# Optimization experiments

Measured on AMD Instinct MI355X. Metric: run time of the kernel, lower is better.

## Reference

```python
import jax, jax.numpy as jnp
import numpy as np

Nc, Ns, Nt, d_h, BS = 64, 64, 64, 128, 16


def setup_inputs() -> dict:
    key = jax.random.key(0)
    k1, k2, k3, k4, k5 = jax.random.split(key, 5)
    Ac = (jax.random.uniform(k1, (Ns, Nc)) < 0.05).astype(jnp.float32)
    As = (jax.random.uniform(k2, (Ns, Ns)) < 0.05).astype(jnp.float32)
    # AA = As@As@Ac + As@Ac + Ac, then binarize (masked_fill(AA != 0, 1))
    AA = As @ As @ Ac + As @ Ac + Ac
    AA = (AA != 0).astype(jnp.float32)                 # [Ns, Nc]
    AA_mask = jnp.tile(AA, (Nt, Nt))                   # [Ns*Nt, Nc*Nt], == AA.repeat(Nt,Nt) in torch
    GCW = jax.random.normal(k3, (Ns * Nt, Nc * Nt), dtype=jnp.float32)
    GCB = jax.random.normal(k4, (Ns * Nt, d_h), dtype=jnp.float32)
    h = jax.random.normal(k5, (BS, Nc, Nt, d_h), dtype=jnp.float32)
    e = jnp.zeros((1,), jnp.float32)                   # unused in forward (kept for signature parity)
    return {"h": h, "e": e, "AA_mask": AA_mask, "GCW": GCW, "GCB": GCB}


def reference(h, e, AA_mask, GCW, GCB):
    bs = h.shape[0]
    # A = relu(AA.repeat(Nt,Nt) * GCW)  -- structured masked weight [Ns*Nt, Nc*Nt]
    A = jax.nn.relu(AA_mask * GCW)
    # h: [bs, Nc, Nt, d_h] -> [bs, Nt, Nc, d_h] -> [bs, Nt*Nc, d_h]
    x = jnp.transpose(h, (0, 2, 1, 3)).reshape(bs, Nt * Nc, d_h)
    # relu(A @ x + GCB): [bs, Ns*Nt, d_h]
    x = jax.nn.relu(jnp.einsum('ij,bjd->bid', A, x) + GCB)
    # [bs, Nt, Ns, d_h] -> [bs, Ns, Nt, d_h] (final torch reshape is a no-op)
    x = x.reshape(bs, Nt, Ns, d_h)
    x = jnp.transpose(x, (0, 2, 1, 3))
    return x
```

## Files before the change

### kernel.cpp

```cpp
#include <hip/hip_runtime.h>


#define NC 64
#define NS 64
#define NT 64
#define DH 128
#define BATCH 16
#define MDIM 4096
#define KDIM 4096
#define TM 128
#define TK 64

typedef __attribute__((ext_vector_type(8))) short short8;
typedef __attribute__((ext_vector_type(4))) float floatx4;

__device__ __forceinline__ unsigned short f2bf(float f) {
    union { float f; unsigned int i; } v; v.f = f;
    return (unsigned short)((v.i + 0x7fffu + ((v.i >> 16) & 1u)) >> 16);
}
__device__ __forceinline__ void async16(const void* g, void* l) {
    __builtin_amdgcn_global_load_lds(
        (const __attribute__((address_space(1))) void*)g,
        (__attribute__((address_space(3))) void*)l, 16, 0, 0);
}

__global__ __launch_bounds__(256)
void prep_a(const float* __restrict__ aam, const float* __restrict__ gcw,
            unsigned short* __restrict__ Abf)
{
    const size_t idx = ((size_t)blockIdx.x * 256 + threadIdx.x) * 8;
    floatx4 a0 = *(const floatx4*)(aam + idx);
    floatx4 a1 = *(const floatx4*)(aam + idx + 4);
    floatx4 w0 = *(const floatx4*)(gcw + idx);
    floatx4 w1 = *(const floatx4*)(gcw + idx + 4);
    short8 p;
#pragma unroll
    for (int e = 0; e < 4; ++e) {
        float v0 = a0[e] * w0[e]; v0 = v0 > 0.f ? v0 : 0.f;
        float v1 = a1[e] * w1[e]; v1 = v1 > 0.f ? v1 : 0.f;
        p[e]     = (short)f2bf(v0);
        p[e + 4] = (short)f2bf(v1);
    }
    *(short8*)(Abf + idx) = p;
}

__global__ __launch_bounds__(256)
void prep_x(const float* __restrict__ hmat, unsigned short* __restrict__ XT)
{
    const int b = blockIdx.x >> 6;
    const int t = blockIdx.x & 63;
    const int tid = threadIdx.x;
    const int d = tid & 127;
    const int half = tid >> 7;
#pragma unroll
    for (int cc = 0; cc < 4; ++cc) {
        const int c0 = half * 32 + cc * 8;
        short8 p;
#pragma unroll
        for (int e = 0; e < 8; ++e) {
            float v = hmat[(((size_t)b * NC + (c0 + e)) * NT + t) * DH + d];
            p[e] = (short)f2bf(v);
        }
        *(short8*)(XT + ((size_t)(b * DH + d)) * KDIM + t * 64 + c0) = p;
    }
}

__global__ __launch_bounds__(256, 2)
void gemm(const unsigned short* __restrict__ Abf,
          const unsigned short* __restrict__ XT,
          const float* __restrict__ gcb,
          float* __restrict__ out)
{
    __shared__ short sA[TM * TK];
    __shared__ short sX[TM * TK];

    const int tid = threadIdx.x;
    const int bid = blockIdx.x;
    const int mp  = (bid & 7) * 4 + (bid >> 7);
    const int b   = (bid >> 3) & 15;
    const int i0  = mp * TM;

    const int lane = tid & 63;
    const int w    = tid >> 6;
    const int wm = (w >> 1) * 64;
    const int wn = (w & 1) * 64;
    const int l15 = lane & 15;
    const int q   = lane >> 4;

    const int srow = lane >> 3;
    const int schk = lane & 7;

    floatx4 acc[4][4];
#pragma unroll
    for (int mi = 0; mi < 4; ++mi)
#pragma unroll
        for (int ni = 0; ni < 4; ++ni)
            acc[mi][ni] = (floatx4){0.f, 0.f, 0.f, 0.f};

    for (int k0 = 0; k0 < KDIM; k0 += TK) {
        __syncthreads();
#pragma unroll
        for (int is = 0; is < 4; ++is) {
            const int r  = w * 8 + is * 32 + srow;
            const int kk = k0 + ((schk ^ (r & 7)) << 3);
            async16(Abf + (size_t)(i0 + r) * KDIM + kk, &sA[(w * 8 + is * 32) * TK]);
            async16(XT  + (size_t)(b * DH + r) * KDIM + kk, &sX[(w * 8 + is * 32) * TK]);
        }
        __syncthreads();

#pragma unroll
        for (int h = 0; h < 2; ++h) {
            short8 af[4], bf[4];
#pragma unroll
            for (int mi = 0; mi < 4; ++mi) {
                const int row = wm + mi * 16 + l15;
                af[mi] = *(const short8*)&sA[row * TK + (((h * 4 + q) ^ (l15 & 7)) << 3)];
            }
#pragma unroll
            for (int ni = 0; ni < 4; ++ni) {
                const int row = wn + ni * 16 + l15;
                bf[ni] = *(const short8*)&sX[row * TK + (((h * 4 + q) ^ (l15 & 7)) << 3)];
            }
#pragma unroll
            for (int mi = 0; mi < 4; ++mi)
#pragma unroll
                for (int ni = 0; ni < 4; ++ni)
                    acc[mi][ni] = __builtin_amdgcn_mfma_f32_16x16x32_bf16(
                        af[mi], bf[ni], acc[mi][ni], 0, 0, 0);
        }
    }

#pragma unroll
    for (int mi = 0; mi < 4; ++mi) {
        const int ibase = i0 + wm + mi * 16 + q * 4;
#pragma unroll
        for (int ni = 0; ni < 4; ++ni) {
            const int d = wn + ni * 16 + l15;
#pragma unroll
            for (int r = 0; r < 4; ++r) {
                const int i = ibase + r;
                float v = acc[mi][ni][r] + gcb[(size_t)i * DH + d];
                v = v > 0.f ? v : 0.f;
                out[(((size_t)b * NS + (i & 63)) * NT + (i >> 6)) * DH + d] = v;
            }
        }
    }
}

#define APAD 40
#define XPAD 20
__global__ __launch_bounds__(256, 2)
void gcn_fused(const float* __restrict__ hmat, const float* __restrict__ aam,
               const float* __restrict__ gcw, const float* __restrict__ gcb,
               float* __restrict__ out)
{
    __shared__ short sA[TM * APAD];
    __shared__ unsigned int sX[DH * XPAD];
    const int tid = threadIdx.x;
    const int bid = blockIdx.x;
    const int mp  = (bid & 7) * 4 + (bid >> 7);
    const int b   = (bid >> 3) & 15;
    const int i0  = mp * TM;
    const int lane = tid & 63;
    const int wm = ((tid >> 6) >> 1) * 64;
    const int wn = ((tid >> 6) & 1) * 64;
    const int l15 = lane & 15;
    const int q   = lane >> 4;
    floatx4 acc[4][4];
#pragma unroll
    for (int mi = 0; mi < 4; ++mi)
#pragma unroll
        for (int ni = 0; ni < 4; ++ni) acc[mi][ni] = (floatx4){0.f,0.f,0.f,0.f};
    const int ar = tid >> 2, ac = (tid & 3) << 3;
    const int kp = tid >> 4, dg = (tid & 15) << 3;
    const int wkey = (tid & 3) << 2;
    for (int k0 = 0; k0 < KDIM; k0 += 32) {
        const size_t ga0 = (size_t)(i0 + ar) * KDIM + (k0 + ac);
        const size_t ga1 = ga0 + (size_t)64 * KDIM;
        floatx4 aa0a = *(const floatx4*)(aam + ga0), aa0b = *(const floatx4*)(aam + ga0 + 4);
        floatx4 ww0a = *(const floatx4*)(gcw + ga0), ww0b = *(const floatx4*)(gcw + ga0 + 4);
        floatx4 aa1a = *(const floatx4*)(aam + ga1), aa1b = *(const floatx4*)(aam + ga1 + 4);
        floatx4 ww1a = *(const floatx4*)(gcw + ga1), ww1b = *(const floatx4*)(gcw + ga1 + 4);
        const int jj = k0 + 2 * kp, tt = jj >> 6, cc = jj & 63;
        const size_t gx0 = ((size_t)(b * NC + cc) * NT + tt) * DH + dg;
        const size_t gx1 = gx0 + (size_t)NT * DH;
        floatx4 x0a = *(const floatx4*)(hmat + gx0), x0b = *(const floatx4*)(hmat + gx0 + 4);
        floatx4 x1a = *(const floatx4*)(hmat + gx1), x1b = *(const floatx4*)(hmat + gx1 + 4);
        __syncthreads();
        short8 p0, p1;
#pragma unroll
        for (int e = 0; e < 4; ++e) {
            float v0 = aa0a[e]*ww0a[e]; v0 = v0>0.f?v0:0.f;
            float v1 = aa0b[e]*ww0b[e]; v1 = v1>0.f?v1:0.f;
            float v2 = aa1a[e]*ww1a[e]; v2 = v2>0.f?v2:0.f;
            float v3 = aa1b[e]*ww1b[e]; v3 = v3>0.f?v3:0.f;
            p0[e] = (short)f2bf(v0); p0[e+4] = (short)f2bf(v1);
            p1[e] = (short)f2bf(v2); p1[e+4] = (short)f2bf(v3);
        }
        *(short8*)&sA[ar * APAD + ac] = p0;
        *(short8*)&sA[(ar + 64) * APAD + ac] = p1;
#pragma unroll
        for (int e = 0; e < 4; ++e) {
            unsigned int pka = (unsigned int)f2bf(x0a[e]) | ((unsigned int)f2bf(x1a[e]) << 16);
            unsigned int pkb = (unsigned int)f2bf(x0b[e]) | ((unsigned int)f2bf(x1b[e]) << 16);
            sX[(dg + e) * XPAD + (kp ^ wkey)] = pka;
            sX[(dg + e + 4) * XPAD + (kp ^ wkey)] = pkb;
        }
        __syncthreads();
        short8 afrag[4], bfrag[4];
#pragma unroll
        for (int mi = 0; mi < 4; ++mi)
            afrag[mi] = *(const short8*)&sA[(wm + mi * 16 + l15) * APAD + q * 8];
#pragma unroll
        for (int ni = 0; ni < 4; ++ni) {
            const int row = wn + ni * 16 + l15;
            const int col = (q * 4) ^ (((row >> 3) & 3) << 2);
            bfrag[ni] = *(const short8*)(sX + row * XPAD + col);
        }
#pragma unroll
        for (int mi = 0; mi < 4; ++mi)
#pragma unroll
            for (int ni = 0; ni < 4; ++ni)
                acc[mi][ni] = __builtin_amdgcn_mfma_f32_16x16x32_bf16(
                    afrag[mi], bfrag[ni], acc[mi][ni], 0, 0, 0);
    }
#pragma unroll
    for (int mi = 0; mi < 4; ++mi) {
        const int ibase = i0 + wm + mi * 16 + q * 4;
#pragma unroll
        for (int ni = 0; ni < 4; ++ni) {
            const int d = wn + ni * 16 + l15;
#pragma unroll
            for (int r = 0; r < 4; ++r) {
                const int i = ibase + r;
                float v = acc[mi][ni][r] + gcb[(size_t)i * DH + d];
                v = v > 0.f ? v : 0.f;
                out[(((size_t)b * NS + (i & 63)) * NT + (i >> 6)) * DH + d] = v;
            }
        }
    }
}

extern "C" void kernel_launch(void* const* d_in, const int* in_sizes, int n_in,
                              void* d_out, int out_size, void* d_ws, size_t ws_size,
                              hipStream_t stream) {
    const float* h   = (const float*)d_in[0];
    const float* aam = (const float*)d_in[2];
    const float* gcw = (const float*)d_in[3];
    const float* gcb = (const float*)d_in[4];
    float* out = (float*)d_out;

    const size_t A_BYTES  = (size_t)MDIM * KDIM * 2;
    const size_t XT_BYTES = (size_t)BATCH * DH * KDIM * 2;

    if (ws_size >= A_BYTES + XT_BYTES) {
        unsigned short* Abf = (unsigned short*)d_ws;
        unsigned short* XT  = (unsigned short*)((char*)d_ws + A_BYTES);
        prep_a<<<dim3((MDIM * KDIM) / (256 * 8)), 256, 0, stream>>>(aam, gcw, Abf);
        prep_x<<<dim3(BATCH * NT), 256, 0, stream>>>(h, XT);
        gemm<<<dim3((MDIM / TM) * BATCH), 256, 0, stream>>>(Abf, XT, gcb, out);
    } else {
        gcn_fused<<<dim3((MDIM / TM) * BATCH), 256, 0, stream>>>(h, aam, gcw, gcb, out);
    }
}
```

Before: 267.4 us.

## Switch GEMM to 32x32x16 MFMA and merge prep kernels into one launch

The GEMM inner loop now uses 32x32x16 bf16 MFMA with 2x2 tiles per wave instead of 16x16x32 with 4x4 tiles, and the epilogue row mapping is updated to match. This halves the number of LDS fragment reads per MFMA and may raise matrix-core throughput. The two preprocessing kernels are merged into one launch that splits on block index, which removes one kernel launch and lets the two jobs overlap. The larger MFMA changes the register layout and the epilogue store pattern, which could affect coalescing of the output writes.

```diff
diff --git a/kernel.cpp b/kernel.cpp
--- a/kernel.cpp
+++ b/kernel.cpp
@@ -13,6 +13,7 @@
 
 typedef __attribute__((ext_vector_type(8))) short short8;
 typedef __attribute__((ext_vector_type(4))) float floatx4;
+typedef __attribute__((ext_vector_type(16))) float floatx16;
 
 __device__ __forceinline__ unsigned short f2bf(float f) {
     union { float f; unsigned int i; } v; v.f = f;
@@ -25,43 +26,44 @@
 }
 
 __global__ __launch_bounds__(256)
-void prep_a(const float* __restrict__ aam, const float* __restrict__ gcw,
-            unsigned short* __restrict__ Abf)
+void prep(const float* __restrict__ aam, const float* __restrict__ gcw,
+          const float* __restrict__ hmat,
+          unsigned short* __restrict__ Abf, unsigned short* __restrict__ XT)
 {
-    const size_t idx = ((size_t)blockIdx.x * 256 + threadIdx.x) * 8;
-    floatx4 a0 = *(const floatx4*)(aam + idx);
-    floatx4 a1 = *(const floatx4*)(aam + idx + 4);
-    floatx4 w0 = *(const floatx4*)(gcw + idx);
-    floatx4 w1 = *(const floatx4*)(gcw + idx + 4);
-    short8 p;
-#pragma unroll
-    for (int e = 0; e < 4; ++e) {
-        float v0 = a0[e] * w0[e]; v0 = v0 > 0.f ? v0 : 0.f;
-        float v1 = a1[e] * w1[e]; v1 = v1 > 0.f ? v1 : 0.f;
-        p[e]     = (short)f2bf(v0);
-        p[e + 4] = (short)f2bf(v1);
-    }
-    *(short8*)(Abf + idx) = p;
-}
-
-__global__ __launch_bounds__(256)
-void prep_x(const float* __restrict__ hmat, unsigned short* __restrict__ XT)
-{
-    const int b = blockIdx.x >> 6;
-    const int t = blockIdx.x & 63;
-    const int tid = threadIdx.x;
-    const int d = tid & 127;
-    const int half = tid >> 7;
-#pragma unroll
-    for (int cc = 0; cc < 4; ++cc) {
-        const int c0 = half * 32 + cc * 8;
+    const int bid = blockIdx.x;
+    if (bid < (MDIM * KDIM) / (256 * 8)) {
+        const size_t idx = ((size_t)bid * 256 + threadIdx.x) * 8;
+        floatx4 a0 = *(const floatx4*)(aam + idx);
+        floatx4 a1 = *(const floatx4*)(aam + idx + 4);
+        floatx4 w0 = *(const floatx4*)(gcw + idx);
+        floatx4 w1 = *(const floatx4*)(gcw + idx + 4);
         short8 p;
 #pragma unroll
-        for (int e = 0; e < 8; ++e) {
-            float v = hmat[(((size_t)b * NC + (c0 + e)) * NT + t) * DH + d];
-            p[e] = (short)f2bf(v);
-        }
-        *(short8*)(XT + ((size_t)(b * DH + d)) * KDIM + t * 64 + c0) = p;
+        for (int e = 0; e < 4; ++e) {
+            float v0 = a0[e] * w0[e]; v0 = v0 > 0.f ? v0 : 0.f;
+            float v1 = a1[e] * w1[e]; v1 = v1 > 0.f ? v1 : 0.f;
+            p[e]     = (short)f2bf(v0);
+            p[e + 4] = (short)f2bf(v1);
+        }
+        *(short8*)(Abf + idx) = p;
+    } else {
+        const int xb = bid - (MDIM * KDIM) / (256 * 8);
+        const int b = xb >> 6;
+        const int t = xb & 63;
+        const int tid = threadIdx.x;
+        const int d = tid & 127;
+        const int half = tid >> 7;
+#pragma unroll
+        for (int cc = 0; cc < 4; ++cc) {
+            const int c0 = half * 32 + cc * 8;
+            short8 p;
+#pragma unroll
+            for (int e = 0; e < 8; ++e) {
+                float v = hmat[(((size_t)b * NC + (c0 + e)) * NT + t) * DH + d];
+                p[e] = (short)f2bf(v);
+            }
+            *(short8*)(XT + ((size_t)(b * DH + d)) * KDIM + t * 64 + c0) = p;
+        }
     }
 }
 
@@ -84,18 +86,20 @@
     const int w    = tid >> 6;
     const int wm = (w >> 1) * 64;
     const int wn = (w & 1) * 64;
-    const int l15 = lane & 15;
-    const int q   = lane >> 4;
+    const int l31  = lane & 31;
+    const int half = lane >> 5;
 
     const int srow = lane >> 3;
     const int schk = lane & 7;
 
-    floatx4 acc[4][4];
-#pragma unroll
-    for (int mi = 0; mi < 4; ++mi)
-#pragma unroll
-        for (int ni = 0; ni < 4; ++ni)
-            acc[mi][ni] = (floatx4){0.f, 0.f, 0.f, 0.f};
+    floatx16 acc[2][2];
+#pragma unroll
+    for (int mt = 0; mt < 2; ++mt)
+#pragma unroll
+        for (int nt = 0; nt < 2; ++nt)
+#pragma unroll
+            for (int r = 0; r < 16; ++r)
+                acc[mt][nt][r] = 0.f;
 
     for (int k0 = 0; k0 < KDIM; k0 += TK) {
         __syncthreads();
@@ -109,42 +113,42 @@
         __syncthreads();
 
 #pragma unroll
-        for (int h = 0; h < 2; ++h) {
-            short8 af[4], bf[4];
-#pragma unroll
-            for (int mi = 0; mi < 4; ++mi) {
-                const int row = wm + mi * 16 + l15;
-                af[mi] = *(const short8*)&sA[row * TK + (((h * 4 + q) ^ (l15 & 7)) << 3)];
-            }
-#pragma unroll
-            for (int ni = 0; ni < 4; ++ni) {
-                const int row = wn + ni * 16 + l15;
-                bf[ni] = *(const short8*)&sX[row * TK + (((h * 4 + q) ^ (l15 & 7)) << 3)];
-            }
-#pragma unroll
-            for (int mi = 0; mi < 4; ++mi)
-#pragma unroll
-                for (int ni = 0; ni < 4; ++ni)
-                    acc[mi][ni] = __builtin_amdgcn_mfma_f32_16x16x32_bf16(
-                        af[mi], bf[ni], acc[mi][ni], 0, 0, 0);
-        }
-    }
-
-#pragma unroll
-    for (int mi = 0; mi < 4; ++mi) {
-        const int ibase = i0 + wm + mi * 16 + q * 4;
-#pragma unroll
-        for (int ni = 0; ni < 4; ++ni) {
-            const int d = wn + ni * 16 + l15;
-#pragma unroll
-            for (int r = 0; r < 4; ++r) {
-                const int i = ibase + r;
-                float v = acc[mi][ni][r] + gcb[(size_t)i * DH + d];
+        for (int h = 0; h < 4; ++h) {
+            const int g = h * 2 + half;
+            short8 af[2], bf[2];
+#pragma unroll
+            for (int mt = 0; mt < 2; ++mt) {
+                const int row = wm + mt * 32 + l31;
+                af[mt] = *(const short8*)&sA[row * TK + ((g ^ (l31 & 7)) << 3)];
+            }
+#pragma unroll
+            for (int nt = 0; nt < 2; ++nt) {
+                const int row = wn + nt * 32 + l31;
+                bf[nt] = *(const short8*)&sX[row * TK + ((g ^ (l31 & 7)) << 3)];
+            }
+#pragma unroll
+            for (int mt = 0; mt < 2; ++mt)
+#pragma unroll
+                for (int nt = 0; nt < 2; ++nt)
+                    acc[mt][nt] = __builtin_amdgcn_mfma_f32_32x32x16_bf16(
+                        af[mt], bf[nt], acc[mt][nt], 0, 0, 0);
+        }
+    }
+
+#pragma unroll
+    for (int mt = 0; mt < 2; ++mt)
+#pragma unroll
+        for (int nt = 0; nt < 2; ++nt) {
+            const int d = wn + nt * 32 + l31;
+#pragma unroll
+            for (int r = 0; r < 16; ++r) {
+                const int row = wm + mt * 32 + (r & 3) + 8 * (r >> 2) + 4 * half;
+                const int i = i0 + row;
+                float v = acc[mt][nt][r] + gcb[(size_t)i * DH + d];
                 v = v > 0.f ? v : 0.f;
                 out[(((size_t)b * NS + (i & 63)) * NT + (i >> 6)) * DH + d] = v;
             }
         }
-    }
 }
 
 #define APAD 40
@@ -256,8 +260,7 @@
     if (ws_size >= A_BYTES + XT_BYTES) {
         unsigned short* Abf = (unsigned short*)d_ws;
         unsigned short* XT  = (unsigned short*)((char*)d_ws + A_BYTES);
-        prep_a<<<dim3((MDIM * KDIM) / (256 * 8)), 256, 0, stream>>>(aam, gcw, Abf);
-        prep_x<<<dim3(BATCH * NT), 256, 0, stream>>>(h, XT);
+        prep<<<dim3((MDIM * KDIM) / (256 * 8) + BATCH * NT), 256, 0, stream>>>(aam, gcw, h, Abf, XT);
         gemm<<<dim3((MDIM / TM) * BATCH), 256, 0, stream>>>(Abf, XT, gcb, out);
     } else {
         gcn_fused<<<dim3((MDIM / TM) * BATCH), 256, 0, stream>>>(h, aam, gcw, gcb, out);
```

New measurement: 271.5 us. About the same (+1.5%).

## Pre-swizzle A into MFMA fragment layout, load from global, double-buffer X

Applied to the files above, without the earlier changes.

The A-matrix prep now writes bf16 A in a fragment-ordered layout so the GEMM can load A operands directly from global/L2 into registers, bypassing LDS. X tiles are double-buffered in LDS with the next tile prefetched asynchronously, halving per-iteration barriers. The two prep kernels are merged into one launch. This trades LDS traffic and syncs for direct global loads of A, which may expose latency since they are not prefetched.

```diff
diff --git a/kernel.cpp b/kernel.cpp
--- a/kernel.cpp
+++ b/kernel.cpp
@@ -25,54 +25,63 @@
 }
 
 __global__ __launch_bounds__(256)
-void prep_a(const float* __restrict__ aam, const float* __restrict__ gcw,
-            unsigned short* __restrict__ Abf)
+void prep(const float* __restrict__ aam, const float* __restrict__ gcw,
+          const float* __restrict__ hmat,
+          unsigned short* __restrict__ A2, unsigned short* __restrict__ XT)
 {
-    const size_t idx = ((size_t)blockIdx.x * 256 + threadIdx.x) * 8;
-    floatx4 a0 = *(const floatx4*)(aam + idx);
-    floatx4 a1 = *(const floatx4*)(aam + idx + 4);
-    floatx4 w0 = *(const floatx4*)(gcw + idx);
-    floatx4 w1 = *(const floatx4*)(gcw + idx + 4);
-    short8 p;
-#pragma unroll
-    for (int e = 0; e < 4; ++e) {
-        float v0 = a0[e] * w0[e]; v0 = v0 > 0.f ? v0 : 0.f;
-        float v1 = a1[e] * w1[e]; v1 = v1 > 0.f ? v1 : 0.f;
-        p[e]     = (short)f2bf(v0);
-        p[e + 4] = (short)f2bf(v1);
-    }
-    *(short8*)(Abf + idx) = p;
-}
-
-__global__ __launch_bounds__(256)
-void prep_x(const float* __restrict__ hmat, unsigned short* __restrict__ XT)
-{
-    const int b = blockIdx.x >> 6;
-    const int t = blockIdx.x & 63;
-    const int tid = threadIdx.x;
-    const int d = tid & 127;
-    const int half = tid >> 7;
-#pragma unroll
-    for (int cc = 0; cc < 4; ++cc) {
-        const int c0 = half * 32 + cc * 8;
-        short8 p;
-#pragma unroll
-        for (int e = 0; e < 8; ++e) {
-            float v = hmat[(((size_t)b * NC + (c0 + e)) * NT + t) * DH + d];
-            p[e] = (short)f2bf(v);
-        }
-        *(short8*)(XT + ((size_t)(b * DH + d)) * KDIM + t * 64 + c0) = p;
+    const int bid = blockIdx.x;
+    if (bid < 2048) {
+        const int mpb = bid >> 6;
+        const int kcg = bid & 63;
+        const int r   = threadIdx.x >> 1;
+        const int kh  = threadIdx.x & 1;
+        const size_t gbase = (size_t)(mpb * 128 + r) * KDIM + kcg * 64 + kh * 32;
+        floatx4 a[8], w[8];
+#pragma unroll
+        for (int c = 0; c < 8; ++c) {
+            a[c] = *(const floatx4*)(aam + gbase + c * 4);
+            w[c] = *(const floatx4*)(gcw + gbase + c * 4);
+        }
+#pragma unroll
+        for (int kc4 = 0; kc4 < 4; ++kc4) {
+            short8 p;
+#pragma unroll
+            for (int e = 0; e < 4; ++e) {
+                float v0 = a[kc4 * 2][e] * w[kc4 * 2][e];         v0 = v0 > 0.f ? v0 : 0.f;
+                float v1 = a[kc4 * 2 + 1][e] * w[kc4 * 2 + 1][e]; v1 = v1 > 0.f ? v1 : 0.f;
+                p[e]     = (short)f2bf(v0);
+                p[e + 4] = (short)f2bf(v1);
+            }
+            const int kc = kcg * 8 + kh * 4 + kc4;
+            *(short8*)(A2 + ((size_t)(mpb * 512 + kc) * 128 + r) * 8) = p;
+        }
+    } else {
+        const int xb = bid - 2048;
+        const int b = xb >> 6;
+        const int t = xb & 63;
+        const int d = threadIdx.x & 127;
+        const int half = threadIdx.x >> 7;
+#pragma unroll
+        for (int cc = 0; cc < 4; ++cc) {
+            const int c0 = half * 32 + cc * 8;
+            short8 p;
+#pragma unroll
+            for (int e = 0; e < 8; ++e) {
+                float v = hmat[(((size_t)b * NC + (c0 + e)) * NT + t) * DH + d];
+                p[e] = (short)f2bf(v);
+            }
+            *(short8*)(XT + ((size_t)(b * DH + d)) * KDIM + t * 64 + c0) = p;
+        }
     }
 }
 
 __global__ __launch_bounds__(256, 2)
-void gemm(const unsigned short* __restrict__ Abf,
+void gemm(const unsigned short* __restrict__ A2,
           const unsigned short* __restrict__ XT,
           const float* __restrict__ gcb,
           float* __restrict__ out)
 {
-    __shared__ short sA[TM * TK];
-    __shared__ short sX[TM * TK];
+    __shared__ short sX[2][TM * TK];
 
     const int tid = threadIdx.x;
     const int bid = blockIdx.x;
@@ -90,6 +99,8 @@
     const int srow = lane >> 3;
     const int schk = lane & 7;
 
+    const size_t afbase = ((size_t)mp * 512 + q) * 1024 + (size_t)(wm + l15) * 8;
+
     floatx4 acc[4][4];
 #pragma unroll
     for (int mi = 0; mi < 4; ++mi)
@@ -97,37 +108,52 @@
         for (int ni = 0; ni < 4; ++ni)
             acc[mi][ni] = (floatx4){0.f, 0.f, 0.f, 0.f};
 
+#pragma unroll
+    for (int is = 0; is < 4; ++is) {
+        const int r  = w * 8 + is * 32 + srow;
+        const int kk = (schk ^ (r & 7)) << 3;
+        async16(XT + (size_t)(b * DH + r) * KDIM + kk, &sX[0][(w * 8 + is * 32) * TK]);
+    }
+
+    int p = 0;
     for (int k0 = 0; k0 < KDIM; k0 += TK) {
         __syncthreads();
-#pragma unroll
-        for (int is = 0; is < 4; ++is) {
-            const int r  = w * 8 + is * 32 + srow;
-            const int kk = k0 + ((schk ^ (r & 7)) << 3);
-            async16(Abf + (size_t)(i0 + r) * KDIM + kk, &sA[(w * 8 + is * 32) * TK]);
-            async16(XT  + (size_t)(b * DH + r) * KDIM + kk, &sX[(w * 8 + is * 32) * TK]);
-        }
-        __syncthreads();
-
-#pragma unroll
-        for (int h = 0; h < 2; ++h) {
-            short8 af[4], bf[4];
-#pragma unroll
-            for (int mi = 0; mi < 4; ++mi) {
-                const int row = wm + mi * 16 + l15;
-                af[mi] = *(const short8*)&sA[row * TK + (((h * 4 + q) ^ (l15 & 7)) << 3)];
-            }
+
+        if (k0 + TK < KDIM) {
+#pragma unroll
+            for (int is = 0; is < 4; ++is) {
+                const int r  = w * 8 + is * 32 + srow;
+                const int kk = k0 + TK + ((schk ^ (r & 7)) << 3);
+                async16(XT + (size_t)(b * DH + r) * KDIM + kk,
+                        &sX[p ^ 1][(w * 8 + is * 32) * TK]);
+            }
+        }
+
+        const short* sxp = sX[p];
+        const unsigned short* ap = A2 + afbase + (size_t)k0 * 128;
+
+        short8 af[2][4], bf[2][4];
+#pragma unroll
+        for (int h = 0; h < 2; ++h)
+#pragma unroll
+            for (int mi = 0; mi < 4; ++mi)
+                af[h][mi] = *(const short8*)(ap + h * 4096 + mi * 128);
+#pragma unroll
+        for (int h = 0; h < 2; ++h)
 #pragma unroll
             for (int ni = 0; ni < 4; ++ni) {
                 const int row = wn + ni * 16 + l15;
-                bf[ni] = *(const short8*)&sX[row * TK + (((h * 4 + q) ^ (l15 & 7)) << 3)];
-            }
+                bf[h][ni] = *(const short8*)&sxp[row * TK + (((h * 4 + q) ^ (l15 & 7)) << 3)];
+            }
+#pragma unroll
+        for (int h = 0; h < 2; ++h)
 #pragma unroll
             for (int mi = 0; mi < 4; ++mi)
 #pragma unroll
                 for (int ni = 0; ni < 4; ++ni)
                     acc[mi][ni] = __builtin_amdgcn_mfma_f32_16x16x32_bf16(
-                        af[mi], bf[ni], acc[mi][ni], 0, 0, 0);
-        }
+                        af[h][mi], bf[h][ni], acc[mi][ni], 0, 0, 0);
+        p ^= 1;
     }
 
 #pragma unroll
@@ -254,11 +280,10 @@
     const size_t XT_BYTES = (size_t)BATCH * DH * KDIM * 2;
 
     if (ws_size >= A_BYTES + XT_BYTES) {
-        unsigned short* Abf = (unsigned short*)d_ws;
-        unsigned short* XT  = (unsigned short*)((char*)d_ws + A_BYTES);
-        prep_a<<<dim3((MDIM * KDIM) / (256 * 8)), 256, 0, stream>>>(aam, gcw, Abf);
-        prep_x<<<dim3(BATCH * NT), 256, 0, stream>>>(h, XT);
-        gemm<<<dim3((MDIM / TM) * BATCH), 256, 0, stream>>>(Abf, XT, gcb, out);
+        unsigned short* A2 = (unsigned short*)d_ws;
+        unsigned short* XT = (unsigned short*)((char*)d_ws + A_BYTES);
+        prep<<<dim3(2048 + BATCH * NT), 256, 0, stream>>>(aam, gcw, h, A2, XT);
+        gemm<<<dim3((MDIM / TM) * BATCH), 256, 0, stream>>>(A2, XT, gcb, out);
     } else {
         gcn_fused<<<dim3((MDIM / TM) * BATCH), 256, 0, stream>>>(h, aam, gcw, gcb, out);
     }
```

Result: slower. 302.3 us (+13.1%).
